# Kernel tuning notes

Measured on AMD Instinct MI355X. Metric: run time of the kernel, lower is better.

## Reference

```python
import jax, jax.numpy as jnp
import numpy as np

NUM_EXPERTS = 4
HIDDEN = 4096
RANK = 8
ALPHA = 8.0
SCALE = ALPHA / RANK  # = 1.0


def setup_inputs() -> dict:
    key = jax.random.key(0)
    ks = jax.random.split(key, 6)
    B, T, H, E, R = 4, 4096, HIDDEN, NUM_EXPERTS, RANK
    x = jax.random.normal(ks[0], (B, T, H), dtype=jnp.float32)
    # frozen base up-projection (H -> H so base_out + updated is shape-consistent)
    W_up = jax.random.normal(ks[1], (H, H), dtype=jnp.float32) / np.sqrt(H)
    gate_w = jax.random.normal(ks[2], (E, H), dtype=jnp.float32) / np.sqrt(H)
    expert_bias = jnp.zeros((E,), dtype=jnp.float32)
    # LoRA params per expert: A [E, R, H], B [E, H, R] (B typically init 0; use small random for a nontrivial test)
    lora_A = jax.random.normal(ks[3], (E, R, H), dtype=jnp.float32) / np.sqrt(H)
    lora_B = jax.random.normal(ks[4], (E, H, R), dtype=jnp.float32) * 0.01
    return {"x": x, "W_up": W_up, "gate_w": gate_w, "expert_bias": expert_bias,
            "lora_A": lora_A, "lora_B": lora_B}


def reference(x, W_up, gate_w, expert_bias, lora_A, lora_B):
    B, T, H = x.shape
    E = gate_w.shape[0]
    x_flat = x.reshape(-1, H)                                  # [N, H]
    logits = x_flat @ gate_w.T + expert_bias                   # [N, E]
    top1 = jnp.argmax(logits, axis=-1)                         # argmax(softmax)==argmax(logits)
    one_hot = jax.nn.one_hot(top1, E, dtype=x_flat.dtype)      # [N, E]
    base_out = jnp.einsum('bth,oh->bto', x, W_up)              # frozen up-proj [B,T,H]
    # LoRA for all experts (rank is tiny), then select the routed expert.
    z = jnp.einsum('nh,erh->ner', x_flat, lora_A)              # [N, E, R]
    d = jnp.einsum('ner,ehr->neh', z, lora_B) * SCALE          # [N, E, H]
    delta = jnp.einsum('neh,ne->nh', d, one_hot)               # [N, H]
    return base_out + delta.reshape(B, T, H)
```

## Files before the change

kernel.cpp:

```cpp
#include <hip/hip_runtime.h>

constexpr int kB = 4;
constexpr int kT = 4096;
constexpr int kN_TOK = kB * kT;
constexpr int kH = 4096;
constexpr int kE = 4;
constexpr int kR = 8;
constexpr float kSCALE = 1.0f;

typedef __bf16 bf16x8 __attribute__((ext_vector_type(8)));
typedef float  f32x4  __attribute__((ext_vector_type(4)));

template <int N> struct IC { static constexpr int value = N; };


__device__ inline unsigned short f2bf(float f) {
  union { float f; unsigned u; } v; v.f = f;
  unsigned r = v.u + 0x7FFFu + ((v.u >> 16) & 1u);
  return (unsigned short)(r >> 16);
}

__device__ inline unsigned pack2(float lo, float hi) {
  return (unsigned)f2bf(lo) | ((unsigned)f2bf(hi) << 16);
}

__device__ inline void gload_lds16(const unsigned short* g, unsigned short* l) {
  __builtin_amdgcn_global_load_lds(
      (const __attribute__((address_space(1))) unsigned int*)g,
      (__attribute__((address_space(3))) unsigned int*)l, 16, 0, 0);
}


__global__ __launch_bounds__(256) void convert_w_kernel(
    const float* __restrict__ w, unsigned short* __restrict__ wb) {
  size_t i = ((size_t)blockIdx.x * 256 + threadIdx.x) * 8;
  float4 a = *(const float4*)(w + i);
  float4 b = *(const float4*)(w + i + 4);
  uint4 s;
  s.x = pack2(a.x, a.y); s.y = pack2(a.z, a.w);
  s.z = pack2(b.x, b.y); s.w = pack2(b.z, b.w);
  *(uint4*)(wb + i) = s;
}


__global__ __launch_bounds__(256) void route_kernel(
    const float* __restrict__ x, const float* __restrict__ gate_w,
    const float* __restrict__ ebias, const float* __restrict__ lora_A,
    unsigned short* __restrict__ xb, float* __restrict__ zbuf,
    int* __restrict__ top1) {
  const int n = blockIdx.x;
  const int t = threadIdx.x;
  const int lane = t & 63, wave = t >> 6;
  const float* xr = x + (size_t)n * kH;

  float4 xv[4];
#pragma unroll
  for (int k = 0; k < 4; ++k) xv[k] = *(const float4*)(xr + k * 1024 + t * 4);

#pragma unroll
  for (int k = 0; k < 4; ++k) {
    uint2 p;
    p.x = pack2(xv[k].x, xv[k].y);
    p.y = pack2(xv[k].z, xv[k].w);
    *(uint2*)(xb + (size_t)n * kH + k * 1024 + t * 4) = p;
  }

  double g[kE];
#pragma unroll
  for (int e = 0; e < kE; ++e) {
    float p = 0.f;
#pragma unroll
    for (int k = 0; k < 4; ++k) {
      float4 w = *(const float4*)(gate_w + (size_t)e * kH + k * 1024 + t * 4);
      p += xv[k].x * w.x + xv[k].y * w.y + xv[k].z * w.z + xv[k].w * w.w;
    }
    g[e] = (double)p;
  }
#pragma unroll
  for (int e = 0; e < kE; ++e)
    for (int off = 32; off; off >>= 1) g[e] += __shfl_down(g[e], off, 64);

  __shared__ double gs[4][kE];
  __shared__ int se;
  if (lane == 0) {
#pragma unroll
    for (int e = 0; e < kE; ++e) gs[wave][e] = g[e];
  }
  __syncthreads();
  if (t == 0) {
    double best = -1e300; int bi = 0;
#pragma unroll
    for (int e = 0; e < kE; ++e) {
      double v = gs[0][e] + gs[1][e] + gs[2][e] + gs[3][e] + (double)ebias[e];
      if (v > best) { best = v; bi = e; }
    }
    se = bi;
    top1[n] = bi;
  }
  __syncthreads();
  const int e = se;

  const float* Ae = lora_A + (size_t)e * kR * kH;
  float zr[kR] = {0, 0, 0, 0, 0, 0, 0, 0};
#pragma unroll
  for (int r = 0; r < kR; ++r) {
#pragma unroll
    for (int k = 0; k < 4; ++k) {
      float4 w = *(const float4*)(Ae + (size_t)r * kH + k * 1024 + t * 4);
      zr[r] += xv[k].x * w.x + xv[k].y * w.y + xv[k].z * w.z + xv[k].w * w.w;
    }
  }
#pragma unroll
  for (int r = 0; r < kR; ++r)
    for (int off = 32; off; off >>= 1) zr[r] += __shfl_down(zr[r], off, 64);

  __shared__ float zs[4][kR];
  if (lane == 0) {
#pragma unroll
    for (int r = 0; r < kR; ++r) zs[wave][r] = zr[r];
  }
  __syncthreads();
  if (t < kR) zbuf[(size_t)n * kR + t] = zs[0][t] + zs[1][t] + zs[2][t] + zs[3][t];
}


__global__ __launch_bounds__(512) void gemm_kernel(
    const unsigned short* __restrict__ A,
    const unsigned short* __restrict__ Bw,
    const float* __restrict__ zbuf,
    const int* __restrict__ top1,
    const float* __restrict__ loraB,
    float* __restrict__ out) {
  constexpr int BK = 32;
  constexpr int NT = kH / BK;
  __shared__ unsigned short lds[65536];

  const int tid = threadIdx.x;
  const int lane = tid & 63, wave = tid >> 6;
  const int wm = wave >> 2, wn = wave & 3;
  const int lm = lane & 15, lq = lane >> 4;

  const int id = blockIdx.x;
  const int q = id >> 3;
  const int bn = q & 15;
  const int bm = (id & 7) * 8 + (q >> 4);

  const unsigned short* Ab = A + (size_t)(bm * 256) * kH;
  const unsigned short* Bb = Bw + (size_t)(bn * 256) * kH;

  int srow[2], soff[2];
#pragma unroll
  for (int j = 0; j < 2; ++j) {
    const int c = j * 512 + tid, row = c >> 2, slot = c & 3;
    srow[j] = row;
    soff[j] = (slot ^ ((row >> 1) & 3)) * 8;
  }

  int offA[8], offB[4];
#pragma unroll
  for (int m = 0; m < 8; ++m) {
    const int row = wm * 128 + m * 16 + lm;
    offA[m] = row * BK + (lq ^ ((row >> 1) & 3)) * 8;
  }
#pragma unroll
  for (int n = 0; n < 4; ++n) {
    const int row = wn * 64 + n * 16 + lm;
    offB[n] = 8192 + row * BK + (lq ^ ((row >> 1) & 3)) * 8;
  }

  f32x4 acc[8][4];
#pragma unroll
  for (int m = 0; m < 8; ++m)
#pragma unroll
    for (int n = 0; n < 4; ++n) acc[m][n] = (f32x4)0.0f;

  auto stage = [&](int t) {
    const int k0 = t * BK;
    unsigned short* bA = &lds[(t & 3) * 16384];
#pragma unroll
    for (int j = 0; j < 2; ++j) {
      const int c = j * 512 + tid;
      gload_lds16(Ab + (size_t)srow[j] * kH + k0 + soff[j], bA + c * 8);
      gload_lds16(Bb + (size_t)srow[j] * kH + k0 + soff[j], bA + 8192 + c * 8);
    }
  };

  auto kstep = [&](int t, auto VM) {
    asm volatile("s_waitcnt vmcnt(%0)" ::"i"((int)VM.value) : "memory");
    __builtin_amdgcn_sched_barrier(0);
    __builtin_amdgcn_s_barrier();
    __builtin_amdgcn_sched_barrier(0);
    asm volatile("" ::: "memory");
    const unsigned short* buf = &lds[(t & 3) * 16384];
    bf16x8 af[8], bf[4];
#pragma unroll
    for (int m = 0; m < 8; ++m) af[m] = *(const bf16x8*)(buf + offA[m]);
#pragma unroll
    for (int n = 0; n < 4; ++n) bf[n] = *(const bf16x8*)(buf + offB[n]);
    __builtin_amdgcn_s_setprio(1);
#pragma unroll
    for (int m = 0; m < 8; ++m)
#pragma unroll
      for (int n = 0; n < 4; ++n)
        acc[m][n] = __builtin_amdgcn_mfma_f32_16x16x32_bf16(
            af[m], bf[n], acc[m][n], 0, 0, 0);
    __builtin_amdgcn_s_setprio(0);
    asm volatile("s_waitcnt lgkmcnt(0)" ::: "memory");
    __builtin_amdgcn_sched_barrier(0);
    __builtin_amdgcn_s_barrier();
    __builtin_amdgcn_sched_barrier(0);
    asm volatile("" ::: "memory");
  };

  stage(0); stage(1); stage(2);
  int t = 0;
  for (; t < NT - 3; ++t) {
    stage(t + 3);
    kstep(t, IC<12>{});
  }
  kstep(t, IC<8>{}); ++t;
  kstep(t, IC<4>{}); ++t;
  kstep(t, IC<0>{});

  const int rowBase = bm * 256 + wm * 128 + lq * 4;
  const int colBase = bn * 256 + wn * 64 + lm;
#pragma unroll
  for (int mt = 0; mt < 8; ++mt) {
#pragma unroll
    for (int r = 0; r < 4; ++r) {
      const int row = rowBase + mt * 16 + r;
      const int e = top1[row];
      const float4 z0 = *(const float4*)(zbuf + (size_t)row * kR);
      const float4 z1 = *(const float4*)(zbuf + (size_t)row * kR + 4);
      const float* Bp = loraB + (size_t)e * kH * kR;
      float* orow = out + (size_t)row * kH;
#pragma unroll
      for (int nt = 0; nt < 4; ++nt) {
        const int col = colBase + nt * 16;
        const float4 b0 = *(const float4*)(Bp + (size_t)col * kR);
        const float4 b1 = *(const float4*)(Bp + (size_t)col * kR + 4);
        float d = z0.x * b0.x + z0.y * b0.y + z0.z * b0.z + z0.w * b0.w +
                  z1.x * b1.x + z1.y * b1.y + z1.z * b1.z + z1.w * b1.w;
        orow[col] = acc[mt][nt][r] + d * kSCALE;
      }
    }
  }
}


extern "C" void kernel_launch(void* const* d_in, const int* in_sizes, int n_in,
                              void* d_out, int out_size, void* d_ws, size_t ws_size,
                              hipStream_t stream) {
  const float* x   = (const float*)d_in[0];
  const float* Wup = (const float*)d_in[1];
  const float* gw  = (const float*)d_in[2];
  const float* eb  = (const float*)d_in[3];
  const float* lA  = (const float*)d_in[4];
  const float* lB  = (const float*)d_in[5];
  float* out = (float*)d_out;

  char* ws = (char*)d_ws;
  unsigned short* wb = (unsigned short*)ws;
  unsigned short* xb = (unsigned short*)(ws + 33554432);
  float* zbuf        = (float*)(ws + 33554432 + 134217728);
  int* top1          = (int*)(ws + 33554432 + 134217728 + 524288);

  convert_w_kernel<<<dim3((kH * kH) / (256 * 8)), dim3(256), 0, stream>>>(Wup, wb);
  route_kernel<<<dim3(kN_TOK), dim3(256), 0, stream>>>(x, gw, eb, lA, xb, zbuf, top1);
  gemm_kernel<<<dim3((kN_TOK / 256) * (kH / 256)), dim3(512), 0, stream>>>(
      xb, wb, zbuf, top1, lB, out);
}
```

Baseline: 1.160 ms.

## Split LoRA-A projection into MFMA kernel and restructure GEMM K-loop pipelining

Moves the LoRA-A down-projection out of the per-token route kernel into a separate MFMA kernel. That kernel computes z for all four experts from bf16 x and bf16-converted lora_A, then keeps the routed expert's slice. The GEMM main loop is rewritten to use one barrier per k-step instead of two. It splits the A fragments into two halves so LDS reads of the next tile and global prefetch interleave with MFMA work. The cost is an extra launch, lower precision in z (bf16 instead of fp32), and four times the LoRA-A FLOPs, while trimming route-kernel scalar work and GEMM barrier stalls.

```diff
diff --git a/kernel.cpp b/kernel.cpp
--- a/kernel.cpp
+++ b/kernel.cpp
@@ -45,9 +45,8 @@
 
 __global__ __launch_bounds__(256) void route_kernel(
     const float* __restrict__ x, const float* __restrict__ gate_w,
-    const float* __restrict__ ebias, const float* __restrict__ lora_A,
-    unsigned short* __restrict__ xb, float* __restrict__ zbuf,
-    int* __restrict__ top1) {
+    const float* __restrict__ ebias,
+    unsigned short* __restrict__ xb, int* __restrict__ top1) {
   const int n = blockIdx.x;
   const int t = threadIdx.x;
   const int lane = t & 63, wave = t >> 6;
@@ -81,7 +80,6 @@
     for (int off = 32; off; off >>= 1) g[e] += __shfl_down(g[e], off, 64);
 
   __shared__ double gs[4][kE];
-  __shared__ int se;
   if (lane == 0) {
 #pragma unroll
     for (int e = 0; e < kE; ++e) gs[wave][e] = g[e];
@@ -94,33 +92,73 @@
       double v = gs[0][e] + gs[1][e] + gs[2][e] + gs[3][e] + (double)ebias[e];
       if (v > best) { best = v; bi = e; }
     }
-    se = bi;
     top1[n] = bi;
   }
-  __syncthreads();
-  const int e = se;
-
-  const float* Ae = lora_A + (size_t)e * kR * kH;
-  float zr[kR] = {0, 0, 0, 0, 0, 0, 0, 0};
-#pragma unroll
-  for (int r = 0; r < kR; ++r) {
-#pragma unroll
-    for (int k = 0; k < 4; ++k) {
-      float4 w = *(const float4*)(Ae + (size_t)r * kH + k * 1024 + t * 4);
-      zr[r] += xv[k].x * w.x + xv[k].y * w.y + xv[k].z * w.z + xv[k].w * w.w;
-    }
-  }
-#pragma unroll
-  for (int r = 0; r < kR; ++r)
-    for (int off = 32; off; off >>= 1) zr[r] += __shfl_down(zr[r], off, 64);
-
-  __shared__ float zs[4][kR];
-  if (lane == 0) {
-#pragma unroll
-    for (int r = 0; r < kR; ++r) zs[wave][r] = zr[r];
-  }
-  __syncthreads();
-  if (t < kR) zbuf[(size_t)n * kR + t] = zs[0][t] + zs[1][t] + zs[2][t] + zs[3][t];
+}
+
+
+__global__ __launch_bounds__(256) void zall_kernel(
+    const unsigned short* __restrict__ xb,
+    const float* __restrict__ lora_A,
+    const int* __restrict__ top1,
+    float* __restrict__ zbuf) {
+  constexpr int BK = 64;
+  constexpr int NTK = kH / BK;
+  __shared__ unsigned short lsX[64 * BK];
+  __shared__ unsigned short lsA[32 * BK];
+
+  const int tid = threadIdx.x;
+  const int lane = tid & 63, wv = tid >> 6;
+  const int lm = lane & 15, lq = lane >> 4;
+  const int rowBase = blockIdx.x * 64;
+  const unsigned short* Xb = xb + (size_t)rowBase * kH;
+
+  const int c0 = tid, c1 = 256 + tid;
+  const int r0 = c0 >> 3, s0 = ((c0 & 7) ^ (r0 & 7)) * 8;
+  const int r1 = c1 >> 3, s1 = ((c1 & 7) ^ (r1 & 7)) * 8;
+  const int ja = tid >> 3, oa = tid & 7;
+
+  f32x4 a0 = {0.f, 0.f, 0.f, 0.f}, a1 = {0.f, 0.f, 0.f, 0.f};
+
+  for (int t = 0; t < NTK; ++t) {
+    const int k0 = t * BK;
+    __syncthreads();
+    gload_lds16(Xb + (size_t)r0 * kH + k0 + s0, &lsX[c0 * 8]);
+    gload_lds16(Xb + (size_t)r1 * kH + k0 + s1, &lsX[c1 * 8]);
+    {
+      const float* src = lora_A + (size_t)ja * kH + k0 + oa * 8;
+      float4 va = *(const float4*)src;
+      float4 vb = *(const float4*)(src + 4);
+      uint4 s;
+      s.x = pack2(va.x, va.y); s.y = pack2(va.z, va.w);
+      s.z = pack2(vb.x, vb.y); s.w = pack2(vb.z, vb.w);
+      *(uint4*)&lsA[ja * BK + ((oa ^ (ja & 7)) * 8)] = s;
+    }
+    __syncthreads();
+
+    bf16x8 ax[2], bx0[2], bx1[2];
+    const int row = wv * 16 + lm;
+#pragma unroll
+    for (int kf = 0; kf < 2; ++kf) {
+      ax[kf]  = *(const bf16x8*)&lsX[row * BK + (((kf * 4 + lq) ^ (row & 7)) * 8)];
+      bx0[kf] = *(const bf16x8*)&lsA[lm * BK + (((kf * 4 + lq) ^ (lm & 7)) * 8)];
+      const int j1 = 16 + lm;
+      bx1[kf] = *(const bf16x8*)&lsA[j1 * BK + (((kf * 4 + lq) ^ (j1 & 7)) * 8)];
+    }
+#pragma unroll
+    for (int kf = 0; kf < 2; ++kf) {
+      a0 = __builtin_amdgcn_mfma_f32_16x16x32_bf16(ax[kf], bx0[kf], a0, 0, 0, 0);
+      a1 = __builtin_amdgcn_mfma_f32_16x16x32_bf16(ax[kf], bx1[kf], a1, 0, 0, 0);
+    }
+  }
+
+#pragma unroll
+  for (int r = 0; r < 4; ++r) {
+    const int row = rowBase + wv * 16 + lq * 4 + r;
+    const int e = top1[row];
+    if ((lm >> 3) == e)        zbuf[(size_t)row * kR + (lm & 7)] = a0[r];
+    if (((16 + lm) >> 3) == e) zbuf[(size_t)row * kR + (lm & 7)] = a1[r];
+  }
 }
 
 
@@ -174,6 +212,8 @@
 #pragma unroll
     for (int n = 0; n < 4; ++n) acc[m][n] = (f32x4)0.0f;
 
+  bf16x8 af0[4], af1[4], bf[4];
+
   auto stage = [&](int t) {
     const int k0 = t * BK;
     unsigned short* bA = &lds[(t & 3) * 16384];
@@ -185,42 +225,66 @@
     }
   };
 
-  auto kstep = [&](int t, auto VM) {
-    asm volatile("s_waitcnt vmcnt(%0)" ::"i"((int)VM.value) : "memory");
+  auto readQ0 = [&](const unsigned short* buf) {
+#pragma unroll
+    for (int n = 0; n < 4; ++n) bf[n] = *(const bf16x8*)(buf + offB[n]);
+#pragma unroll
+    for (int m = 0; m < 4; ++m) af0[m] = *(const bf16x8*)(buf + offA[m]);
+  };
+  auto readQ1 = [&](const unsigned short* buf) {
+#pragma unroll
+    for (int m = 0; m < 4; ++m) af1[m] = *(const bf16x8*)(buf + offA[4 + m]);
+  };
+
+  auto kstep = [&](int t, auto VM, auto STAGE, auto NEXT) {
+    const unsigned short* buf = &lds[(t & 3) * 16384];
+    readQ1(buf);
     __builtin_amdgcn_sched_barrier(0);
-    __builtin_amdgcn_s_barrier();
-    __builtin_amdgcn_sched_barrier(0);
-    asm volatile("" ::: "memory");
-    const unsigned short* buf = &lds[(t & 3) * 16384];
-    bf16x8 af[8], bf[4];
-#pragma unroll
-    for (int m = 0; m < 8; ++m) af[m] = *(const bf16x8*)(buf + offA[m]);
-#pragma unroll
-    for (int n = 0; n < 4; ++n) bf[n] = *(const bf16x8*)(buf + offB[n]);
     __builtin_amdgcn_s_setprio(1);
 #pragma unroll
-    for (int m = 0; m < 8; ++m)
+    for (int m = 0; m < 4; ++m)
 #pragma unroll
       for (int n = 0; n < 4; ++n)
         acc[m][n] = __builtin_amdgcn_mfma_f32_16x16x32_bf16(
-            af[m], bf[n], acc[m][n], 0, 0, 0);
+            af0[m], bf[n], acc[m][n], 0, 0, 0);
     __builtin_amdgcn_s_setprio(0);
-    asm volatile("s_waitcnt lgkmcnt(0)" ::: "memory");
     __builtin_amdgcn_sched_barrier(0);
-    __builtin_amdgcn_s_barrier();
+    if constexpr (STAGE.value) stage(t + 3);
     __builtin_amdgcn_sched_barrier(0);
-    asm volatile("" ::: "memory");
+    __builtin_amdgcn_s_setprio(1);
+#pragma unroll
+    for (int m = 0; m < 4; ++m)
+#pragma unroll
+      for (int n = 0; n < 4; ++n)
+        acc[4 + m][n] = __builtin_amdgcn_mfma_f32_16x16x32_bf16(
+            af1[m], bf[n], acc[4 + m][n], 0, 0, 0);
+    __builtin_amdgcn_s_setprio(0);
+    __builtin_amdgcn_sched_barrier(0);
+    if constexpr (NEXT.value) {
+      asm volatile("s_waitcnt vmcnt(%0)" ::"i"((int)VM.value) : "memory");
+      __builtin_amdgcn_sched_barrier(0);
+      __builtin_amdgcn_s_barrier();
+      __builtin_amdgcn_sched_barrier(0);
+      asm volatile("" ::: "memory");
+      readQ0(&lds[((t + 1) & 3) * 16384]);
+      __builtin_amdgcn_sched_barrier(0);
+    }
   };
 
   stage(0); stage(1); stage(2);
+  asm volatile("s_waitcnt vmcnt(8)" ::: "memory");
+  __builtin_amdgcn_sched_barrier(0);
+  __builtin_amdgcn_s_barrier();
+  __builtin_amdgcn_sched_barrier(0);
+  asm volatile("" ::: "memory");
+  readQ0(&lds[0]);
+  __builtin_amdgcn_sched_barrier(0);
+
   int t = 0;
-  for (; t < NT - 3; ++t) {
-    stage(t + 3);
-    kstep(t, IC<12>{});
-  }
-  kstep(t, IC<8>{}); ++t;
-  kstep(t, IC<4>{}); ++t;
-  kstep(t, IC<0>{});
+  for (; t < NT - 3; ++t) kstep(t, IC<8>{}, IC<1>{}, IC<1>{});
+  kstep(t, IC<4>{}, IC<0>{}, IC<1>{}); ++t;
+  kstep(t, IC<0>{}, IC<0>{}, IC<1>{}); ++t;
+  kstep(t, IC<0>{}, IC<0>{}, IC<0>{});
 
   const int rowBase = bm * 256 + wm * 128 + lq * 4;
   const int colBase = bn * 256 + wn * 64 + lm;
@@ -266,7 +330,8 @@
   int* top1          = (int*)(ws + 33554432 + 134217728 + 524288);
 
   convert_w_kernel<<<dim3((kH * kH) / (256 * 8)), dim3(256), 0, stream>>>(Wup, wb);
-  route_kernel<<<dim3(kN_TOK), dim3(256), 0, stream>>>(x, gw, eb, lA, xb, zbuf, top1);
+  route_kernel<<<dim3(kN_TOK), dim3(256), 0, stream>>>(x, gw, eb, xb, top1);
+  zall_kernel<<<dim3(kN_TOK / 64), dim3(256), 0, stream>>>(xb, lA, top1, zbuf);
   gemm_kernel<<<dim3((kN_TOK / 256) * (kH / 256)), dim3(512), 0, stream>>>(
       xb, wb, zbuf, top1, lB, out);
 }
```

Measured after the change: 1.088 ms. -6.3%, faster.
